# Performance work log

Hardware: AMD Instinct MI355X
Metric: run time of the kernel (lower is better)

Reference implementation:

```python
import jax, jax.numpy as jnp
import numpy as np

D_MODEL = 1024
N_HEADS = 16
D_K = D_MODEL // N_HEADS
THETA = 10000.0
BATCH = 2
SEQ = 2048


def apply_rope(x, positions):
    # x: [B, H, S, d_k], positions: [S] int
    half = D_K // 2
    inv_freq = 1.0 / (THETA ** (jnp.arange(half, dtype=jnp.float32) * 2.0 / D_K))  # [half]
    ang = positions.astype(jnp.float32)[:, None] * inv_freq[None, :]  # [S, half]
    cos = jnp.cos(ang)
    sin = jnp.sin(ang)
    xr = x.reshape(x.shape[:-1] + (half, 2))
    x1, x2 = xr[..., 0], xr[..., 1]
    o1 = x1 * cos - x2 * sin
    o2 = x1 * sin + x2 * cos
    return jnp.stack([o1, o2], axis=-1).reshape(x.shape)


def setup_inputs() -> dict:
    key = jax.random.key(0)
    ks = jax.random.split(key, 5)
    scale = 1.0 / np.sqrt(D_MODEL)
    return {
        "x": jax.random.normal(ks[0], (BATCH, SEQ, D_MODEL), jnp.float32),
        "token_positions": jnp.arange(SEQ, dtype=jnp.int32),
        "Wq": jax.random.normal(ks[1], (D_MODEL, D_MODEL), jnp.float32) * scale,
        "Wk": jax.random.normal(ks[2], (D_MODEL, D_MODEL), jnp.float32) * scale,
        "Wv": jax.random.normal(ks[3], (D_MODEL, D_MODEL), jnp.float32) * scale,
        "Wo": jax.random.normal(ks[4], (D_MODEL, D_MODEL), jnp.float32) * scale,
    }


def reference(x, token_positions, Wq, Wk, Wv, Wo):
    B, S, _ = x.shape
    # projections (Linear with weight [out, in], no bias): y = x @ W^T
    def split_heads(t):
        return t.reshape(B, S, N_HEADS, D_K).transpose(0, 2, 1, 3)  # [B,H,S,d_k]

    Q = split_heads(x @ Wq.T)
    K = split_heads(x @ Wk.T)
    V = split_heads(x @ Wv.T)

    Q = apply_rope(Q, token_positions)
    K = apply_rope(K, token_positions)

    scores = jnp.einsum("bhqd,bhkd->bhqk", Q, K) / np.sqrt(D_K)
    causal = jnp.tril(jnp.ones((S, S), dtype=bool))
    scores = jnp.where(causal, scores, -jnp.inf)
    attn = jax.nn.softmax(scores, axis=-1)
    out = jnp.einsum("bhqk,bhkd->bhqd", attn, V)  # [B,H,S,d_k]
    out = out.transpose(0, 2, 1, 3).reshape(B, S, D_MODEL)
    return out @ Wo.T
```

## Files before the change

kernel.cpp:

```cpp
#include <hip/hip_runtime.h>
#include <hip/hip_bf16.h>


typedef __bf16 bf16x8 __attribute__((ext_vector_type(8)));
typedef __bf16 bf16x4 __attribute__((ext_vector_type(4)));
typedef float f32x4 __attribute__((ext_vector_type(4)));
typedef unsigned short ushort8 __attribute__((ext_vector_type(8)));

#define BATCH 2
#define SEQ 2048
#define NH 16
#define DK 64
#define DM 1024
#define BH (BATCH*NH)
#define M_TOT (BATCH*SEQ)
#define NQT (SEQ/64)

__device__ __forceinline__ void gload16(const void* g, void* l) {
    __builtin_amdgcn_global_load_lds((const __attribute__((address_space(1))) void*)g,
                                     (__attribute__((address_space(3))) void*)l, 16, 0, 0);
}

__global__ void cvt_kernel(const float* __restrict__ s, __bf16* __restrict__ d, int n) {
    int i = (blockIdx.x * blockDim.x + threadIdx.x) * 4;
    if (i >= n) return;
    float4 v = *(const float4*)(s + i);
    bf16x4 o;
    o[0] = (__bf16)v.x; o[1] = (__bf16)v.y; o[2] = (__bf16)v.z; o[3] = (__bf16)v.w;
    *(bf16x4*)(d + i) = o;
}

__global__ void cvt4_kernel(const float* __restrict__ s0, const float* __restrict__ s1,
                            const float* __restrict__ s2, const float* __restrict__ s3,
                            __bf16* __restrict__ d0, __bf16* __restrict__ d1,
                            __bf16* __restrict__ d2, __bf16* __restrict__ d3, int n) {
    const int z = blockIdx.y;
    const float* s = (z == 0) ? s0 : (z == 1) ? s1 : (z == 2) ? s2 : s3;
    __bf16* d = (z == 0) ? d0 : (z == 1) ? d1 : (z == 2) ? d2 : d3;
    int i = (blockIdx.x * blockDim.x + threadIdx.x) * 4;
    if (i >= n) return;
    float4 v = *(const float4*)(s + i);
    bf16x4 o;
    o[0] = (__bf16)v.x; o[1] = (__bf16)v.y; o[2] = (__bf16)v.z; o[3] = (__bf16)v.w;
    *(bf16x4*)(d + i) = o;
}

__device__ __forceinline__ void gemm_tile_compute(
    const __bf16* __restrict__ A, const __bf16* __restrict__ W,
    int m0, int n0, int K, __bf16* sA, __bf16* sB, f32x4 (&acc)[4][4])
{
    const int t = threadIdx.x;
    const int lane = t & 63, wid = t >> 6;
    const int wr = wid >> 1, wc = wid & 1;
    const int g = lane >> 4, l15 = lane & 15;

    f32x4 zero = {0.f, 0.f, 0.f, 0.f};
#pragma unroll
    for (int mt = 0; mt < 4; ++mt)
#pragma unroll
        for (int nt = 0; nt < 4; ++nt) acc[mt][nt] = zero;

    for (int k0 = 0; k0 < K; k0 += 32) {
        __syncthreads();
#pragma unroll
        for (int rnd = 0; rnd < 2; ++rnd) {
            int s = rnd * 256 + t;
            int row = s >> 2, ch = s & 3;
            __bf16* dstA = sA + (rnd * 256 + wid * 64) * 8;
            __bf16* dstB = sB + (rnd * 256 + wid * 64) * 8;
            gload16(A + (size_t)(m0 + row) * K + k0 + ch * 8, dstA);
            gload16(W + (size_t)(n0 + row) * K + k0 + ch * 8, dstB);
        }
        __syncthreads();
        bf16x8 af[4], bfr[4];
#pragma unroll
        for (int mt = 0; mt < 4; ++mt)
            af[mt] = *(const bf16x8*)&sA[(wr * 64 + mt * 16 + l15) * 32 + g * 8];
#pragma unroll
        for (int nt = 0; nt < 4; ++nt)
            bfr[nt] = *(const bf16x8*)&sB[(wc * 64 + nt * 16 + l15) * 32 + g * 8];
#pragma unroll
        for (int mt = 0; mt < 4; ++mt)
#pragma unroll
            for (int nt = 0; nt < 4; ++nt)
                acc[mt][nt] = __builtin_amdgcn_mfma_f32_16x16x32_bf16(af[mt], bfr[nt], acc[mt][nt], 0, 0, 0);
    }
}

__global__ __launch_bounds__(256) void gemm_qkv(
    const __bf16* __restrict__ xb,
    const __bf16* __restrict__ wq, const __bf16* __restrict__ wk, const __bf16* __restrict__ wv,
    __bf16* __restrict__ Qb, __bf16* __restrict__ Kb, __bf16* __restrict__ VTb)
{
    __shared__ __align__(16) __bf16 sA[128 * 32], sB[128 * 32];
    const int z = blockIdx.z;
    const __bf16* W = (z == 0) ? wq : ((z == 1) ? wk : wv);
    f32x4 acc[4][4];
    const int m0 = blockIdx.y * 128, n0 = blockIdx.x * 128;
    gemm_tile_compute(xb, W, m0, n0, DM, sA, sB, acc);

    const int t = threadIdx.x, lane = t & 63, wid = t >> 6;
    const int wr = wid >> 1, wc = wid & 1, g = lane >> 4, l15 = lane & 15;
    __bf16* QK = (z == 0) ? Qb : Kb;
#pragma unroll
    for (int mt = 0; mt < 4; ++mt)
#pragma unroll
        for (int nt = 0; nt < 4; ++nt)
#pragma unroll
            for (int r = 0; r < 4; ++r) {
                int m = m0 + wr * 64 + mt * 16 + g * 4 + r;
                int n = n0 + wc * 64 + nt * 16 + l15;
                int b = m >> 11, s = m & 2047, h = n >> 6, d = n & 63;
                __bf16 v = (__bf16)acc[mt][nt][r];
                if (z < 2)
                    QK[(((size_t)(b * NH + h)) * SEQ + s) * DK + d] = v;
                else
                    VTb[(((size_t)(b * NH + h)) * DK + d) * SEQ + s] = v;
            }
}

__global__ __launch_bounds__(256) void gemm_out(
    const __bf16* __restrict__ AO, const __bf16* __restrict__ wo, float* __restrict__ out)
{
    __shared__ __align__(16) __bf16 sA[128 * 32], sB[128 * 32];
    f32x4 acc[4][4];
    const int m0 = blockIdx.y * 128, n0 = blockIdx.x * 128;
    gemm_tile_compute(AO, wo, m0, n0, DM, sA, sB, acc);

    const int t = threadIdx.x, lane = t & 63, wid = t >> 6;
    const int wr = wid >> 1, wc = wid & 1, g = lane >> 4, l15 = lane & 15;
#pragma unroll
    for (int mt = 0; mt < 4; ++mt)
#pragma unroll
        for (int nt = 0; nt < 4; ++nt)
#pragma unroll
            for (int r = 0; r < 4; ++r) {
                int m = m0 + wr * 64 + mt * 16 + g * 4 + r;
                int n = n0 + wc * 64 + nt * 16 + l15;
                out[(size_t)m * DM + n] = acc[mt][nt][r];
            }
}

__global__ __launch_bounds__(256) void rope_kernel(
    __bf16* __restrict__ Qb, __bf16* __restrict__ Kb, const int* __restrict__ pos)
{
    __shared__ float ctab[32], stab[32];
    const int s = blockIdx.x;
    const int t = threadIdx.x;
    if (t < 32) {
        float invf = exp2f(-13.287712379549449f * (float)t * (1.0f / 32.0f));
        float ang = (float)pos[s] * invf;
        float sn, cs;
        sincosf(ang, &sn, &cs);
        ctab[t] = cs; stab[t] = sn;
    }
    __syncthreads();
#pragma unroll
    for (int u = 0; u < 8; ++u) {
        int id = u * 256 + t;
        int i = id & 31;
        int bh = (id >> 5) & 31;
        __bf16* P = (id >> 10) ? Kb : Qb;
        __bf16* p = P + ((size_t)bh * SEQ + s) * DK + i * 2;
        float x1 = (float)p[0], x2 = (float)p[1];
        float c = ctab[i], sn = stab[i];
        p[0] = (__bf16)(x1 * c - x2 * sn);
        p[1] = (__bf16)(x1 * sn + x2 * c);
    }
}

__global__ __launch_bounds__(256) void attn_kernel(
    const __bf16* __restrict__ Qb, const __bf16* __restrict__ Kb,
    const __bf16* __restrict__ VTb, __bf16* __restrict__ AO)
{
    __shared__ __align__(16) __bf16 sK[64 * 64];
    __shared__ __align__(16) __bf16 sV[64 * 64];
    __shared__ __align__(16) __bf16 sP[4 * 16 * 64];

    const int x = blockIdx.x, bh = blockIdx.y;
    const int t = threadIdx.x, lane = t & 63, wid = t >> 6;
    const int g = lane >> 4, l15 = lane & 15;

    const size_t baseQK = (size_t)bh * SEQ * DK;
    const size_t baseVT = (size_t)bh * DK * SEQ;
    const int b = bh >> 4, h = bh & 15;

    char* myP = (char*)(sP + wid * 16 * 64);
    f32x4 zero = {0.f, 0.f, 0.f, 0.f};

    for (int ph = 0; ph < 2; ++ph) {
        const int qt = ph ? (NQT - 1 - x) : x;

        bf16x8 qf[2];
        {
            const __bf16* qp = Qb + baseQK + (size_t)(qt * 64 + wid * 16 + l15) * DK;
            qf[0] = *(const bf16x8*)(qp + g * 8);
            qf[1] = *(const bf16x8*)(qp + 32 + g * 8);
        }

        f32x4 oacc[4];
#pragma unroll
        for (int dt = 0; dt < 4; ++dt) oacc[dt] = zero;
        float mrow[4], lrow[4];
#pragma unroll
        for (int r = 0; r < 4; ++r) { mrow[r] = -3e38f; lrow[r] = 0.f; }

        const char* Kt0 = (const char*)(Kb + baseQK);
        const char* Vt0 = (const char*)(VTb + baseVT);

        for (int kt = 0; kt <= qt; ++kt) {
            __syncthreads();
            const char* Kt = Kt0 + (size_t)kt * 64 * 128;
            const char* Vt = Vt0 + (size_t)kt * 128;
#pragma unroll
            for (int cc = 0; cc < 2; ++cc) {
                int c = t + cc * 256;
                int r = c >> 3, p = c & 7;
                int pp = p ^ (r & 7);
                *(ushort8*)((char*)sK + r * 128 + pp * 16) =
                    *(const ushort8*)(Kt + (size_t)r * 128 + p * 16);
                *(ushort8*)((char*)sV + r * 128 + pp * 16) =
                    *(const ushort8*)(Vt + (size_t)r * (SEQ * 2) + p * 16);
            }
            __syncthreads();

            f32x4 sacc[4];
#pragma unroll
            for (int nt = 0; nt < 4; ++nt) {
                sacc[nt] = zero;
#pragma unroll
                for (int ks = 0; ks < 2; ++ks) {
                    int row = nt * 16 + l15;
                    bf16x8 kf = *(const bf16x8*)((const char*)sK + row * 128 +
                                                 ((ks * 64 + g * 16) ^ ((row & 7) << 4)));
                    sacc[nt] = __builtin_amdgcn_mfma_f32_16x16x32_bf16(qf[ks], kf, sacc[nt], 0, 0, 0);
                }
            }
#pragma unroll
            for (int nt = 0; nt < 4; ++nt)
#pragma unroll
                for (int r = 0; r < 4; ++r) {
                    float sv = sacc[nt][r] * 0.125f;
                    if (kt == qt) {
                        int c_local = nt * 16 + l15;
                        int q_local = wid * 16 + g * 4 + r;
                        if (c_local > q_local) sv = -3e38f;
                    }
                    sacc[nt][r] = sv;
                }

#pragma unroll
            for (int r = 0; r < 4; ++r) {
                float tm = fmaxf(fmaxf(sacc[0][r], sacc[1][r]), fmaxf(sacc[2][r], sacc[3][r]));
#pragma unroll
                for (int msk = 1; msk < 16; msk <<= 1) tm = fmaxf(tm, __shfl_xor(tm, msk));
                float mnew = fmaxf(mrow[r], tm);
                float sc = __expf(mrow[r] - mnew);
                float rs = 0.f;
#pragma unroll
                for (int nt = 0; nt < 4; ++nt) {
                    float p = __expf(sacc[nt][r] - mnew);
                    sacc[nt][r] = p;
                    rs += p;
                }
#pragma unroll
                for (int msk = 1; msk < 16; msk <<= 1) rs += __shfl_xor(rs, msk);
                lrow[r] = lrow[r] * sc + rs;
                mrow[r] = mnew;
#pragma unroll
                for (int dt = 0; dt < 4; ++dt) oacc[dt][r] *= sc;
            }

#pragma unroll
            for (int nt = 0; nt < 4; ++nt)
#pragma unroll
                for (int r = 0; r < 4; ++r) {
                    int row = g * 4 + r;
                    *(__bf16*)(myP + row * 128 +
                               ((nt * 32 + l15 * 2) ^ ((row & 7) << 4))) = (__bf16)sacc[nt][r];
                }

#pragma unroll
            for (int ks = 0; ks < 2; ++ks) {
                bf16x8 pf = *(const bf16x8*)(myP + l15 * 128 +
                                             ((ks * 64 + g * 16) ^ ((l15 & 7) << 4)));
#pragma unroll
                for (int dt = 0; dt < 4; ++dt) {
                    int row = dt * 16 + l15;
                    bf16x8 vf = *(const bf16x8*)((const char*)sV + row * 128 +
                                                 ((ks * 64 + g * 16) ^ ((row & 7) << 4)));
                    oacc[dt] = __builtin_amdgcn_mfma_f32_16x16x32_bf16(pf, vf, oacc[dt], 0, 0, 0);
                }
            }
        }

#pragma unroll
        for (int r = 0; r < 4; ++r) {
            float inv = 1.0f / lrow[r];
            int srow = qt * 64 + wid * 16 + g * 4 + r;
            size_t obase = ((size_t)b * SEQ + srow) * DM + h * DK;
#pragma unroll
            for (int dt = 0; dt < 4; ++dt)
                AO[obase + dt * 16 + l15] = (__bf16)(oacc[dt][r] * inv);
        }
    }
}

extern "C" void kernel_launch(void* const* d_in, const int* in_sizes, int n_in,
                              void* d_out, int out_size, void* d_ws, size_t ws_size,
                              hipStream_t stream) {
    (void)in_sizes; (void)n_in; (void)out_size; (void)ws_size;
    const float* x  = (const float*)d_in[0];
    const int*  pos = (const int*)d_in[1];
    const float* Wq = (const float*)d_in[2];
    const float* Wk = (const float*)d_in[3];
    const float* Wv = (const float*)d_in[4];
    const float* Wo = (const float*)d_in[5];
    float* out = (float*)d_out;

    char* ws = (char*)d_ws;
    __bf16* xb  = (__bf16*)ws; ws += (size_t)M_TOT * DM * 2;
    __bf16* wqb = (__bf16*)ws; ws += (size_t)DM * DM * 2;
    __bf16* wkb = (__bf16*)ws; ws += (size_t)DM * DM * 2;
    __bf16* wvb = (__bf16*)ws; ws += (size_t)DM * DM * 2;
    __bf16* wob = (__bf16*)ws; ws += (size_t)DM * DM * 2;
    __bf16* Qb  = (__bf16*)ws; ws += (size_t)BH * SEQ * DK * 2;
    __bf16* Kb  = (__bf16*)ws; ws += (size_t)BH * SEQ * DK * 2;
    __bf16* VTb = (__bf16*)ws; ws += (size_t)BH * SEQ * DK * 2;
    __bf16* AOb = (__bf16*)ws; ws += (size_t)M_TOT * DM * 2;

    const int nx = M_TOT * DM, nw = DM * DM;
    cvt_kernel<<<nx / 4 / 256, 256, 0, stream>>>(x, xb, nx);
    cvt4_kernel<<<dim3(nw / 4 / 256, 4), 256, 0, stream>>>(Wq, Wk, Wv, Wo, wqb, wkb, wvb, wob, nw);

    gemm_qkv<<<dim3(DM / 128, M_TOT / 128, 3), 256, 0, stream>>>(xb, wqb, wkb, wvb, Qb, Kb, VTb);
    rope_kernel<<<SEQ, 256, 0, stream>>>(Qb, Kb, pos);
    attn_kernel<<<dim3(NQT / 2, BH), 256, 0, stream>>>(Qb, Kb, VTb, AOb);
    gemm_out<<<dim3(DM / 128, M_TOT / 128), 256, 0, stream>>>(AOb, wob, out);
}
```

Measured before the change: 229.4 us.

## Double-buffer attention K/V loads, fuse QKV weights, swizzle blocks across XCDs

The attention kernel now double-buffers K/V tiles in LDS through direct global-to-LDS loads, so the next tile is fetched while the current one is computed. Row sums are reduced only once at the end, and rescaling uses a lazy threshold that skips it unless the row max grows by more than 8. The Q softmax scale is folded into RoPE, and the QKV weights are concatenated into one GEMM. All three GEMM/attention grids are remapped so each XCD works on neighbouring tiles for L2 locality. In exchange the attention kernel uses more LDS and its launch bound now requests two blocks per SM, and the lazy rescale changes numerics slightly.

```diff
diff --git a/kernel.cpp b/kernel.cpp
--- a/kernel.cpp
+++ b/kernel.cpp
@@ -14,7 +14,6 @@
 #define DM 1024
 #define BH (BATCH*NH)
 #define M_TOT (BATCH*SEQ)
-#define NQT (SEQ/64)
 
 __device__ __forceinline__ void gload16(const void* g, void* l) {
     __builtin_amdgcn_global_load_lds((const __attribute__((address_space(1))) void*)g,
@@ -88,20 +87,19 @@
 }
 
 __global__ __launch_bounds__(256) void gemm_qkv(
-    const __bf16* __restrict__ xb,
-    const __bf16* __restrict__ wq, const __bf16* __restrict__ wk, const __bf16* __restrict__ wv,
+    const __bf16* __restrict__ xb, const __bf16* __restrict__ wqkv,
     __bf16* __restrict__ Qb, __bf16* __restrict__ Kb, __bf16* __restrict__ VTb)
 {
     __shared__ __align__(16) __bf16 sA[128 * 32], sB[128 * 32];
-    const int z = blockIdx.z;
-    const __bf16* W = (z == 0) ? wq : ((z == 1) ? wk : wv);
+    int id = blockIdx.x + 24 * blockIdx.y;
+    id = (id & 7) * 96 + (id >> 3);
+    const int m0 = (id / 24) * 128, n0 = (id % 24) * 128;
+
     f32x4 acc[4][4];
-    const int m0 = blockIdx.y * 128, n0 = blockIdx.x * 128;
-    gemm_tile_compute(xb, W, m0, n0, DM, sA, sB, acc);
+    gemm_tile_compute(xb, wqkv, m0, n0, DM, sA, sB, acc);
 
     const int t = threadIdx.x, lane = t & 63, wid = t >> 6;
     const int wr = wid >> 1, wc = wid & 1, g = lane >> 4, l15 = lane & 15;
-    __bf16* QK = (z == 0) ? Qb : Kb;
 #pragma unroll
     for (int mt = 0; mt < 4; ++mt)
 #pragma unroll
@@ -110,10 +108,13 @@
             for (int r = 0; r < 4; ++r) {
                 int m = m0 + wr * 64 + mt * 16 + g * 4 + r;
                 int n = n0 + wc * 64 + nt * 16 + l15;
-                int b = m >> 11, s = m & 2047, h = n >> 6, d = n & 63;
+                int z = n >> 10, hd = n & 1023, h = hd >> 6, d = hd & 63;
+                int b = m >> 11, s = m & 2047;
                 __bf16 v = (__bf16)acc[mt][nt][r];
-                if (z < 2)
-                    QK[(((size_t)(b * NH + h)) * SEQ + s) * DK + d] = v;
+                if (z == 0)
+                    Qb[(((size_t)(b * NH + h)) * SEQ + s) * DK + d] = v;
+                else if (z == 1)
+                    Kb[(((size_t)(b * NH + h)) * SEQ + s) * DK + d] = v;
                 else
                     VTb[(((size_t)(b * NH + h)) * DK + d) * SEQ + s] = v;
             }
@@ -123,8 +124,11 @@
     const __bf16* __restrict__ AO, const __bf16* __restrict__ wo, float* __restrict__ out)
 {
     __shared__ __align__(16) __bf16 sA[128 * 32], sB[128 * 32];
+    int id = blockIdx.x + 8 * blockIdx.y;
+    id = (id & 7) * 32 + (id >> 3);
+    const int m0 = (id / 8) * 128, n0 = (id % 8) * 128;
+
     f32x4 acc[4][4];
-    const int m0 = blockIdx.y * 128, n0 = blockIdx.x * 128;
     gemm_tile_compute(AO, wo, m0, n0, DM, sA, sB, acc);
 
     const int t = threadIdx.x, lane = t & 63, wid = t >> 6;
@@ -160,24 +164,29 @@
         int id = u * 256 + t;
         int i = id & 31;
         int bh = (id >> 5) & 31;
-        __bf16* P = (id >> 10) ? Kb : Qb;
+        int isK = id >> 10;
+        __bf16* P = isK ? Kb : Qb;
+        float qs = isK ? 1.0f : 0.125f;
         __bf16* p = P + ((size_t)bh * SEQ + s) * DK + i * 2;
         float x1 = (float)p[0], x2 = (float)p[1];
         float c = ctab[i], sn = stab[i];
-        p[0] = (__bf16)(x1 * c - x2 * sn);
-        p[1] = (__bf16)(x1 * sn + x2 * c);
+        p[0] = (__bf16)(qs * (x1 * c - x2 * sn));
+        p[1] = (__bf16)(qs * (x1 * sn + x2 * c));
     }
 }
 
-__global__ __launch_bounds__(256) void attn_kernel(
+__global__ __launch_bounds__(256, 2) void attn_kernel(
     const __bf16* __restrict__ Qb, const __bf16* __restrict__ Kb,
     const __bf16* __restrict__ VTb, __bf16* __restrict__ AO)
 {
-    __shared__ __align__(16) __bf16 sK[64 * 64];
-    __shared__ __align__(16) __bf16 sV[64 * 64];
+    __shared__ __align__(16) __bf16 sK[2][64 * 64];
+    __shared__ __align__(16) __bf16 sV[2][64 * 64];
     __shared__ __align__(16) __bf16 sP[4 * 16 * 64];
 
-    const int x = blockIdx.x, bh = blockIdx.y;
+    const int n = blockIdx.x;
+    const int xcd = n & 7, slot = n >> 3;
+    const int bh = xcd * 4 + (slot >> 4);
+    const int x = slot & 15;
     const int t = threadIdx.x, lane = t & 63, wid = t >> 6;
     const int g = lane >> 4, l15 = lane & 15;
 
@@ -185,90 +194,94 @@
     const size_t baseVT = (size_t)bh * DK * SEQ;
     const int b = bh >> 4, h = bh & 15;
 
-    char* myP = (char*)(sP + wid * 16 * 64);
+    const char* Kt0 = (const char*)(Kb + baseQK);
+    const char* Vt0 = (const char*)(VTb + baseVT);
+    char* myP = (char*)sP + wid * 2048;
     f32x4 zero = {0.f, 0.f, 0.f, 0.f};
 
+    auto stage_tile = [&](int kt, int bq) {
+        const char* Kt = Kt0 + (size_t)kt * 64 * 128;
+        const char* Vt = Vt0 + (size_t)kt * 128;
+#pragma unroll
+        for (int cc = 0; cc < 2; ++cc) {
+            int c = t + cc * 256;
+            int r = c >> 3, pp = c & 7;
+            int p = pp ^ (r & 7);
+            char* bK = (char*)sK[bq] + (cc * 256 + wid * 64) * 16;
+            char* bV = (char*)sV[bq] + (cc * 256 + wid * 64) * 16;
+            gload16(Kt + (size_t)r * 128 + p * 16, bK);
+            gload16(Vt + (size_t)r * (SEQ * 2) + p * 16, bV);
+        }
+    };
+
     for (int ph = 0; ph < 2; ++ph) {
-        const int qt = ph ? (NQT - 1 - x) : x;
+        const int j = ph ? (31 - x) : x;
+        const int qrow_w = j * 64 + wid * 16;
+        const int ktmax = j;
 
         bf16x8 qf[2];
         {
-            const __bf16* qp = Qb + baseQK + (size_t)(qt * 64 + wid * 16 + l15) * DK;
+            const __bf16* qp = Qb + baseQK + (size_t)(qrow_w + l15) * DK;
             qf[0] = *(const bf16x8*)(qp + g * 8);
             qf[1] = *(const bf16x8*)(qp + 32 + g * 8);
         }
 
         f32x4 oacc[4];
+        float mrow[4], lacc[4];
 #pragma unroll
         for (int dt = 0; dt < 4; ++dt) oacc[dt] = zero;
-        float mrow[4], lrow[4];
-#pragma unroll
-        for (int r = 0; r < 4; ++r) { mrow[r] = -3e38f; lrow[r] = 0.f; }
-
-        const char* Kt0 = (const char*)(Kb + baseQK);
-        const char* Vt0 = (const char*)(VTb + baseVT);
-
-        for (int kt = 0; kt <= qt; ++kt) {
-            __syncthreads();
-            const char* Kt = Kt0 + (size_t)kt * 64 * 128;
-            const char* Vt = Vt0 + (size_t)kt * 128;
-#pragma unroll
-            for (int cc = 0; cc < 2; ++cc) {
-                int c = t + cc * 256;
-                int r = c >> 3, p = c & 7;
-                int pp = p ^ (r & 7);
-                *(ushort8*)((char*)sK + r * 128 + pp * 16) =
-                    *(const ushort8*)(Kt + (size_t)r * 128 + p * 16);
-                *(ushort8*)((char*)sV + r * 128 + pp * 16) =
-                    *(const ushort8*)(Vt + (size_t)r * (SEQ * 2) + p * 16);
-            }
-            __syncthreads();
+#pragma unroll
+        for (int r = 0; r < 4; ++r) { mrow[r] = -3e38f; lacc[r] = 0.f; }
+
+        stage_tile(0, 0);
+        __syncthreads();
+        int cur = 0;
+
+        for (int kt = 0; kt <= ktmax; ++kt) {
+            if (kt < ktmax) stage_tile(kt + 1, cur ^ 1);
 
             f32x4 sacc[4];
 #pragma unroll
             for (int nt = 0; nt < 4; ++nt) {
                 sacc[nt] = zero;
+                int row = nt * 16 + l15;
 #pragma unroll
                 for (int ks = 0; ks < 2; ++ks) {
-                    int row = nt * 16 + l15;
-                    bf16x8 kf = *(const bf16x8*)((const char*)sK + row * 128 +
+                    bf16x8 kf = *(const bf16x8*)((const char*)sK[cur] + row * 128 +
                                                  ((ks * 64 + g * 16) ^ ((row & 7) << 4)));
                     sacc[nt] = __builtin_amdgcn_mfma_f32_16x16x32_bf16(qf[ks], kf, sacc[nt], 0, 0, 0);
                 }
             }
-#pragma unroll
-            for (int nt = 0; nt < 4; ++nt)
-#pragma unroll
-                for (int r = 0; r < 4; ++r) {
-                    float sv = sacc[nt][r] * 0.125f;
-                    if (kt == qt) {
-                        int c_local = nt * 16 + l15;
-                        int q_local = wid * 16 + g * 4 + r;
-                        if (c_local > q_local) sv = -3e38f;
+
+            if (kt == ktmax) {
+#pragma unroll
+                for (int nt = 0; nt < 4; ++nt)
+#pragma unroll
+                    for (int r = 0; r < 4; ++r) {
+                        int kv = kt * 64 + nt * 16 + l15;
+                        int q = qrow_w + g * 4 + r;
+                        if (kv > q) sacc[nt][r] = -3e38f;
                     }
-                    sacc[nt][r] = sv;
-                }
+            }
 
 #pragma unroll
             for (int r = 0; r < 4; ++r) {
                 float tm = fmaxf(fmaxf(sacc[0][r], sacc[1][r]), fmaxf(sacc[2][r], sacc[3][r]));
 #pragma unroll
                 for (int msk = 1; msk < 16; msk <<= 1) tm = fmaxf(tm, __shfl_xor(tm, msk));
-                float mnew = fmaxf(mrow[r], tm);
-                float sc = __expf(mrow[r] - mnew);
-                float rs = 0.f;
+                if (tm > mrow[r] + 8.0f) {
+                    float sc = __expf(mrow[r] - tm);
+                    mrow[r] = tm;
+                    lacc[r] *= sc;
+#pragma unroll
+                    for (int dt = 0; dt < 4; ++dt) oacc[dt][r] *= sc;
+                }
 #pragma unroll
                 for (int nt = 0; nt < 4; ++nt) {
-                    float p = __expf(sacc[nt][r] - mnew);
+                    float p = __expf(sacc[nt][r] - mrow[r]);
                     sacc[nt][r] = p;
-                    rs += p;
-                }
-#pragma unroll
-                for (int msk = 1; msk < 16; msk <<= 1) rs += __shfl_xor(rs, msk);
-                lrow[r] = lrow[r] * sc + rs;
-                mrow[r] = mnew;
-#pragma unroll
-                for (int dt = 0; dt < 4; ++dt) oacc[dt][r] *= sc;
+                    lacc[r] += p;
+                }
             }
 
 #pragma unroll
@@ -287,17 +300,23 @@
 #pragma unroll
                 for (int dt = 0; dt < 4; ++dt) {
                     int row = dt * 16 + l15;
-                    bf16x8 vf = *(const bf16x8*)((const char*)sV + row * 128 +
+                    bf16x8 vf = *(const bf16x8*)((const char*)sV[cur] + row * 128 +
                                                  ((ks * 64 + g * 16) ^ ((row & 7) << 4)));
                     oacc[dt] = __builtin_amdgcn_mfma_f32_16x16x32_bf16(pf, vf, oacc[dt], 0, 0, 0);
                 }
             }
+
+            __syncthreads();
+            cur ^= 1;
         }
 
 #pragma unroll
         for (int r = 0; r < 4; ++r) {
-            float inv = 1.0f / lrow[r];
-            int srow = qt * 64 + wid * 16 + g * 4 + r;
+            float rs = lacc[r];
+#pragma unroll
+            for (int msk = 1; msk < 16; msk <<= 1) rs += __shfl_xor(rs, msk);
+            float inv = 1.0f / rs;
+            int srow = qrow_w + g * 4 + r;
             size_t obase = ((size_t)b * SEQ + srow) * DM + h * DK;
 #pragma unroll
             for (int dt = 0; dt < 4; ++dt)
@@ -319,22 +338,21 @@
     float* out = (float*)d_out;
 
     char* ws = (char*)d_ws;
-    __bf16* xb  = (__bf16*)ws; ws += (size_t)M_TOT * DM * 2;
-    __bf16* wqb = (__bf16*)ws; ws += (size_t)DM * DM * 2;
-    __bf16* wkb = (__bf16*)ws; ws += (size_t)DM * DM * 2;
-    __bf16* wvb = (__bf16*)ws; ws += (size_t)DM * DM * 2;
-    __bf16* wob = (__bf16*)ws; ws += (size_t)DM * DM * 2;
-    __bf16* Qb  = (__bf16*)ws; ws += (size_t)BH * SEQ * DK * 2;
-    __bf16* Kb  = (__bf16*)ws; ws += (size_t)BH * SEQ * DK * 2;
-    __bf16* VTb = (__bf16*)ws; ws += (size_t)BH * SEQ * DK * 2;
-    __bf16* AOb = (__bf16*)ws; ws += (size_t)M_TOT * DM * 2;
+    __bf16* xb   = (__bf16*)ws; ws += (size_t)M_TOT * DM * 2;
+    __bf16* wqkv = (__bf16*)ws; ws += (size_t)3 * DM * DM * 2;
+    __bf16* wob  = (__bf16*)ws; ws += (size_t)DM * DM * 2;
+    __bf16* Qb   = (__bf16*)ws; ws += (size_t)BH * SEQ * DK * 2;
+    __bf16* Kb   = (__bf16*)ws; ws += (size_t)BH * SEQ * DK * 2;
+    __bf16* VTb  = (__bf16*)ws; ws += (size_t)BH * SEQ * DK * 2;
+    __bf16* AOb  = (__bf16*)ws; ws += (size_t)M_TOT * DM * 2;
 
     const int nx = M_TOT * DM, nw = DM * DM;
     cvt_kernel<<<nx / 4 / 256, 256, 0, stream>>>(x, xb, nx);
-    cvt4_kernel<<<dim3(nw / 4 / 256, 4), 256, 0, stream>>>(Wq, Wk, Wv, Wo, wqb, wkb, wvb, wob, nw);
-
-    gemm_qkv<<<dim3(DM / 128, M_TOT / 128, 3), 256, 0, stream>>>(xb, wqb, wkb, wvb, Qb, Kb, VTb);
+    cvt4_kernel<<<dim3(nw / 4 / 256, 4), 256, 0, stream>>>(
+        Wq, Wk, Wv, Wo, wqkv, wqkv + nw, wqkv + 2 * nw, wob, nw);
+
+    gemm_qkv<<<dim3(24, M_TOT / 128), 256, 0, stream>>>(xb, wqkv, Qb, Kb, VTb);
     rope_kernel<<<SEQ, 256, 0, stream>>>(Qb, Kb, pos);
-    attn_kernel<<<dim3(NQT / 2, BH), 256, 0, stream>>>(Qb, Kb, VTb, AOb);
-    gemm_out<<<dim3(DM / 128, M_TOT / 128), 256, 0, stream>>>(AOb, wob, out);
-}
+    attn_kernel<<<512, 256, 0, stream>>>(Qb, Kb, VTb, AOb);
+    gemm_out<<<dim3(8, M_TOT / 128), 256, 0, stream>>>(AOb, wob, out);
+}
```

Result: faster. 220.3 us (-4.0%).
